# Kernel tuning notes

Hardware: AMD Instinct MI355X
Metric: run time of the kernel (lower is better)

Reference implementation:

```python
import jax, jax.numpy as jnp
import numpy as np

K_SIZE, STRIDE, PAD = 3, 2, 1

def _conv1x1(x, w, b):
    return jnp.einsum('bchw,oc->bohw', x, w) + b[None, :, None, None]

def _unfold(x, k, s, p):
    # Matches torch F.unfold ordering: channel-major, then (kh, kw). -> [B, C, k*k, L]
    B, C, H, W = x.shape
    xp = jnp.pad(x, ((0, 0), (0, 0), (p, p), (p, p)))
    ho = (H + 2 * p - k) // s + 1
    wo = (W + 2 * p - k) // s + 1
    cols = []
    for i in range(k):
        for j in range(k):
            cols.append(xp[:, :, i:i + s * (ho - 1) + 1:s, j:j + s * (wo - 1) + 1:s])
    patches = jnp.stack(cols, axis=2)            # [B, C, k*k, ho, wo]
    return patches.reshape(B, C, k * k, ho * wo)

def _forward(shallow, deep, K_w, K_b, KSA_w, KSA_b):
    B, C, H, W = shallow.shape
    d = (2 * C) // 16
    h, w = H // STRIDE, W // STRIDE
    hw = h * w
    max_out = _conv1x1(deep, KSA_w, KSA_b)            # [B, d, h, w]
    # global re-score branch
    max_out1 = jnp.max(max_out, axis=1)               # [B, h, w]
    q = max_out1.reshape(B, hw)                       # [B, hw]
    kt = max_out.reshape(B, hw, d)                    # faithful to torch .view(B,-1,d) (channel-scrambled flat view)
    lit = jnp.einsum('bp,bpd->bd', q, kt) / hw        # mean over hw of outer products -> [B, d]
    V = max_out.reshape(B, d, hw)
    re_score = jnp.einsum('bd,bdp->bp', lit, V).reshape(B, 1, h, w)
    sig = jax.nn.sigmoid(re_score)
    # local windowed attention branch
    Kx = _conv1x1(shallow, K_w, K_b)                  # [B, out, H, W]
    Kunf = _unfold(Kx, K_SIZE, STRIDE, PAD)           # [B, out, kk, hw]
    # torch does matmul([d,1],[1,kk]) then mean over d == mean_d(q_d) * K patch element
    qmean = jnp.mean(max_out, axis=1).reshape(B, 1, 1, hw)
    logits = qmean * Kunf                             # [B, out, kk, hw]
    new_kernel = jax.nn.softmax(logits, axis=2)       # softmax over window dim kk
    att = jnp.sum(new_kernel * Kunf, axis=2)          # [B, out, hw]
    att = att.reshape(B, -1, h, w)
    return sig * att + att, re_score

def setup_inputs():
    key = jax.random.key(0)
    ks = jax.random.split(key, 6)
    B, C, H, W = 4, 256, 128, 128
    out_c, d = 256, (2 * C) // 16
    return {
        'shallow': jax.random.normal(ks[0], (B, C, H, W), jnp.float32),
        'deep': jax.random.normal(ks[1], (B, 2 * C, H // 2, W // 2), jnp.float32),
        'K_w': jax.random.normal(ks[2], (out_c, C), jnp.float32) * 0.02,
        'K_b': jax.random.normal(ks[3], (out_c,), jnp.float32) * 0.02,
        'KSA_w': jax.random.normal(ks[4], (d, 2 * C), jnp.float32) * 0.02,
        'KSA_b': jax.random.normal(ks[5], (d,), jnp.float32) * 0.02,
    }

def reference(shallow, deep, K_w, K_b, KSA_w, KSA_b):
    return _forward(shallow, deep, K_w, K_b, KSA_w, KSA_b)
```

## Files before the change

kernel.cpp:

```cpp
#include <hip/hip_runtime.h>

typedef unsigned short u16;
typedef __attribute__((ext_vector_type(8))) short short8;
typedef __attribute__((ext_vector_type(4))) float float4v;
typedef __attribute__((ext_vector_type(4))) unsigned short ushort4v;

__device__ __forceinline__ u16 f2bf(float f) {
    unsigned u = __float_as_uint(f);
    u += 0x7FFFu + ((u >> 16) & 1u);
    return (u16)(u >> 16);
}
__device__ __forceinline__ float bf2f(u16 u) {
    return __uint_as_float(((unsigned)u) << 16);
}

__device__ __forceinline__ void lds_barrier() {
    asm volatile("s_waitcnt lgkmcnt(0)\n\ts_barrier" ::: "memory");
}

__device__ float g_maxout[4 * 32 * 4096];
__device__ float g_maxoutT[4 * 4096 * 32];
__device__ float g_q[16384];
__device__ float g_qmean[16384];
__device__ float g_lit[128];
__device__ float g_sigfac[16384];
__device__ u16   g_KwP[65536];
__device__ u16   g_KSAwP[16384];
__device__ u16   g_Kx[4 * 256 * 16384];

__global__ __launch_bounds__(256) void prep_kernel(
    const float* __restrict__ Kw, const float* __restrict__ KSAw)
{
    const int idx = blockIdx.x * 256 + threadIdx.x;
    if (idx < 128) g_lit[idx] = 0.f;
    if (idx < 65536) {
        const int o = idx >> 8, c = idx & 255;
        const int fi = ((o >> 4) << 3) + (c >> 5);
        const int ln = (((c >> 3) & 3) << 4) + (o & 15);
        g_KwP[fi * 512 + ln * 8 + (c & 7)] = f2bf(Kw[idx]);
    }
    if (idx < 16384) {
        const int o = idx >> 9, c = idx & 511;
        const int fi = ((c >> 5) << 1) + (o >> 4);
        const int ln = (((c >> 3) & 3) << 4) + (o & 15);
        g_KSAwP[fi * 512 + ln * 8 + (c & 7)] = f2bf(KSAw[idx]);
    }
}

__global__ __launch_bounds__(256) void gemm_deep(
    const float* __restrict__ Bias, const float* __restrict__ X)
{
    __shared__ u16 As[16384];
    const int t = threadIdx.x;
    const int wave = t >> 6, lane = t & 63;
    const int quad = lane >> 4, n16 = lane & 15;
    const int b = blockIdx.y;
    const int p = blockIdx.x * 64 + wave * 16 + n16;
    const float* Xb = X + ((long long)b << 21) + p;

#pragma unroll
    for (int i = 0; i < 8; i++)
        *(short8*)(As + ((i << 8) + t) * 8) = *(const short8*)(g_KSAwP + ((i << 8) + t) * 8);

    float xr[3][8];
#define DXLOAD(dst, kb_) { \
    const float* xp_ = Xb + ((((kb_) << 5) + (quad << 3)) << 12); \
    _Pragma("unroll") for (int j = 0; j < 8; j++) dst[j] = xp_[j << 12]; }

    DXLOAD(xr[0], 0)
    DXLOAD(xr[1], 1)
    DXLOAD(xr[2], 2)

    __syncthreads();

    float4v acc[2];
#pragma unroll
    for (int i = 0; i < 2; i++) acc[i] = (float4v){0.f, 0.f, 0.f, 0.f};

#pragma unroll
    for (int kb = 0; kb < 16; kb++) {
        short8 bfrag;
#pragma unroll
        for (int j = 0; j < 8; j++) bfrag[j] = (short)f2bf(xr[kb % 3][j]);
        if (kb < 13) DXLOAD(xr[(kb + 3) % 3], kb + 3)
#pragma unroll
        for (int ot = 0; ot < 2; ot++) {
            const short8 afrag = *(const short8*)(As + (((kb << 1) + ot) << 9) + lane * 8);
            acc[ot] = __builtin_amdgcn_mfma_f32_16x16x32_bf16(afrag, bfrag, acc[ot], 0, 0, 0);
        }
    }
#undef DXLOAD

    float mx = -3.4e38f, sm = 0.f;
#pragma unroll
    for (int ot = 0; ot < 2; ot++) {
        float4v vv;
#pragma unroll
        for (int r = 0; r < 4; r++) {
            const int o = ot * 16 + quad * 4 + r;
            vv[r] = acc[ot][r] + Bias[o];
            g_maxout[((b * 32 + o) << 12) + p] = vv[r];
            mx = fmaxf(mx, vv[r]);
            sm += vv[r];
        }
        *(float4v*)(g_maxoutT + (((b << 12) + p) << 5) + ot * 16 + quad * 4) = vv;
    }
    mx = fmaxf(mx, __shfl_xor(mx, 16, 64));
    sm += __shfl_xor(sm, 16, 64);
    mx = fmaxf(mx, __shfl_xor(mx, 32, 64));
    sm += __shfl_xor(sm, 32, 64);
    if (quad == 0) {
        g_q[(b << 12) + p] = mx;
        g_qmean[(b << 12) + p] = sm * (1.f / 32.f);
    }
}

__global__ __launch_bounds__(256) void lit_kernel()
{
    const int b = blockIdx.y;
    const int f0 = blockIdx.x * 1024;
    const int t = threadIdx.x;
    const float* mo = g_maxout + (b << 17);
    const float* qb = g_q + (b << 12);
    float acc = 0.f;
#pragma unroll
    for (int it = 0; it < 4; it++) {
        const int f = f0 + it * 256 + t;
        acc += qb[f >> 5] * mo[f];
    }
    __shared__ float red[256];
    red[t] = acc;
    __syncthreads();
    if (t < 32) {
        float s = 0.f;
#pragma unroll
        for (int k = 0; k < 8; k++) s += red[t + k * 32];
        atomicAdd(&g_lit[b * 32 + t], s * (1.f / 4096.f));
    }
}

__global__ __launch_bounds__(128) void rescore_kernel(float* __restrict__ out_re)
{
    const int idx = blockIdx.x * 128 + threadIdx.x;
    const int b = idx >> 12;
    const float4v* mt = (const float4v*)(g_maxoutT + (idx << 5));
    const float4v* lb = (const float4v*)(g_lit + b * 32);
    float r = 0.f;
#pragma unroll
    for (int j = 0; j < 8; j++) {
        const float4v m4 = mt[j];
        const float4v l4 = lb[j];
        r += m4[0] * l4[0] + m4[1] * l4[1] + m4[2] * l4[2] + m4[3] * l4[3];
    }
    out_re[idx] = r;
    g_sigfac[idx] = 1.f + 1.f / (1.f + __expf(-r));
}

__global__ __launch_bounds__(256) void gemm_kx(
    const float* __restrict__ Bias, const float* __restrict__ X)
{
    __shared__ u16 As[2][8192];
    const int t = threadIdx.x;
    const int wave = t >> 6, lane = t & 63;
    const int quad = lane >> 4, n16 = lane & 15;
    const int b = blockIdx.y;
    const int p0 = blockIdx.x * 64;
    const float* Xb = X + ((long long)b << 22) + p0 + wave * 16 + n16;

    const u16* agbase = g_KwP + wave * 16384 + lane * 8;
    const int alds = wave * 2048 + lane * 8;

    float xr[3][8];
#define XLOAD(dst, kb_) { \
    const float* xp_ = Xb + ((((kb_) << 5) + (quad << 3)) << 14); \
    _Pragma("unroll") for (int j = 0; j < 8; j++) dst[j] = xp_[j << 14]; }

    float4v acc[16];
#pragma unroll
    for (int i = 0; i < 16; i++) acc[i] = (float4v){0.f, 0.f, 0.f, 0.f};

    {
        short8 areg[4];
#pragma unroll
        for (int i = 0; i < 4; i++) areg[i] = *(const short8*)(agbase + i * 4096);
        XLOAD(xr[0], 0)
        XLOAD(xr[1], 1)
        XLOAD(xr[2], 2)
#pragma unroll
        for (int i = 0; i < 4; i++) *(short8*)(&As[0][alds + i * 512]) = areg[i];
    }
    lds_barrier();

#pragma unroll
    for (int kb = 0; kb < 8; kb++) {
        short8 areg[4];
        if (kb < 7) {
#pragma unroll
            for (int i = 0; i < 4; i++)
                areg[i] = *(const short8*)(agbase + i * 4096 + (kb + 1) * 512);
        }
        short8 bfrag;
#pragma unroll
        for (int j = 0; j < 8; j++) bfrag[j] = (short)f2bf(xr[kb % 3][j]);
        if (kb < 5) XLOAD(xr[(kb + 3) % 3], kb + 3)

        const u16* ap = &As[kb & 1][lane * 8];
#pragma unroll
        for (int ot = 0; ot < 16; ot++) {
            const short8 afrag = *(const short8*)(ap + ot * 512);
            acc[ot] = __builtin_amdgcn_mfma_f32_16x16x32_bf16(
                bfrag, afrag, acc[ot], 0, 0, 0);
        }

        if (kb < 7) {
#pragma unroll
            for (int i = 0; i < 4; i++)
                *(short8*)(&As[(kb + 1) & 1][alds + i * 512]) = areg[i];
            lds_barrier();
        }
    }
#undef XLOAD

    u16* kxb = g_Kx + (((long long)b << 8) << 14);
#pragma unroll
    for (int ot = 0; ot < 16; ot++) {
        const int o = ot * 16 + n16;
        const float bo = Bias[o];
        ushort4v w;
#pragma unroll
        for (int r = 0; r < 4; r++) w[r] = f2bf(acc[ot][r] + bo);
        *(ushort4v*)(kxb + ((long long)o << 14) + p0 + wave * 16 + (quad << 2)) = w;
    }
}

__global__ __launch_bounds__(256) void att_window(float* __restrict__ out)
{
    __shared__ u16 tile[8][9][132];
    const int t = threadIdx.x;
    const int o0 = blockIdx.y << 3, b = blockIdx.z;
    const int y0 = (blockIdx.x << 3) - 1;
    const u16* kxb = g_Kx + (((long long)b << 8) << 14);

    if (t < 72) tile[t / 9][t % 9][64] = 0;
#pragma unroll
    for (int k = 0; k < 18; k++) {
        const int e = (k << 8) + t;
        const int row = e >> 6, pr = e & 63;
        const int oi = row / 9, r = row - oi * 9;
        const int y = y0 + r;
        unsigned v = 0;
        if (y >= 0 && y < 128)
            v = *(const unsigned*)(kxb + (((long long)(o0 + oi)) << 14) + (y << 7) + (pr << 1));
        tile[oi][r][pr] = (u16)(v & 0xffffu);
        tile[oi][r][65 + pr] = (u16)(v >> 16);
    }
    __syncthreads();

    const int p = (blockIdx.x << 8) + t;
    const int pw = t & 63;
    const int rl = (t >> 6) << 1;
    const float m = g_qmean[(b << 12) + p];
    const float sf = g_sigfac[(b << 12) + p];

#pragma unroll
    for (int oi = 0; oi < 8; oi++) {
        float v[9];
#pragma unroll
        for (int ki = 0; ki < 3; ++ki) {
            v[ki * 3 + 0] = bf2f(tile[oi][rl + ki][64 + pw]);
            v[ki * 3 + 1] = bf2f(tile[oi][rl + ki][pw]);
            v[ki * 3 + 2] = bf2f(tile[oi][rl + ki][65 + pw]);
        }
        float mx = -3.4e38f;
#pragma unroll
        for (int k = 0; k < 9; ++k) mx = fmaxf(mx, m * v[k]);
        float s = 0.f, a = 0.f;
#pragma unroll
        for (int k = 0; k < 9; ++k) {
            const float e = __expf(m * v[k] - mx);
            s += e;
            a += e * v[k];
        }
        out[((((long long)b << 8) + o0 + oi) << 12) + p] = (a / s) * sf;
    }
}

extern "C" void kernel_launch(void* const* d_in, const int* in_sizes, int n_in,
                              void* d_out, int out_size, void* d_ws, size_t ws_size,
                              hipStream_t stream) {
    const float *shallow = 0, *deep = 0, *K_w = 0, *K_b = 0, *KSA_w = 0, *KSA_b = 0;
    for (int i = 0; i < n_in; ++i) {
        switch (in_sizes[i]) {
            case 16777216: shallow = (const float*)d_in[i]; break;
            case 8388608:  deep    = (const float*)d_in[i]; break;
            case 65536:    K_w     = (const float*)d_in[i]; break;
            case 256:      K_b     = (const float*)d_in[i]; break;
            case 16384:    KSA_w   = (const float*)d_in[i]; break;
            case 32:       KSA_b   = (const float*)d_in[i]; break;
        }
    }
    float* out = (float*)d_out;

    prep_kernel<<<320, 256, 0, stream>>>(K_w, KSA_w);
    gemm_deep<<<dim3(64, 4), 256, 0, stream>>>(KSA_b, deep);
    lit_kernel<<<dim3(128, 4), 256, 0, stream>>>();
    rescore_kernel<<<128, 128, 0, stream>>>(out + 4194304);
    gemm_kx<<<dim3(256, 4), 256, 0, stream>>>(K_b, shallow);
    att_window<<<dim3(16, 32, 4), 256, 0, stream>>>(out);
}
```

Measured before the change: 181.6 us.

## Stage activation tile in LDS and keep weight fragments in registers for Kx GEMM

The Kx 1x1-conv GEMM now loads the block's 64-pixel by 256-channel activation tile with float4 reads, converts it to bf16 once, and stores it in a swizzled LDS buffer. Each wave then owns 64 output channels and keeps its weight fragments in double-buffered registers loaded straight from global memory. This removes the per-k-step LDS barriers and the strided scalar global activation loads of the previous design. In exchange it needs more LDS and accumulator registers, and every wave reads weight fragments from global/L2 instead of sharing them through LDS.

Result: no change. 183.0 us (+0.8%).

```diff
diff --git a/kernel.cpp b/kernel.cpp
--- a/kernel.cpp
+++ b/kernel.cpp
@@ -12,10 +12,6 @@
 }
 __device__ __forceinline__ float bf2f(u16 u) {
     return __uint_as_float(((unsigned)u) << 16);
-}
-
-__device__ __forceinline__ void lds_barrier() {
-    asm volatile("s_waitcnt lgkmcnt(0)\n\ts_barrier" ::: "memory");
 }
 
 __device__ float g_maxout[4 * 32 * 4096];
@@ -159,77 +155,85 @@
 __global__ __launch_bounds__(256) void gemm_kx(
     const float* __restrict__ Bias, const float* __restrict__ X)
 {
-    __shared__ u16 As[2][8192];
+    __shared__ u16 Bs[16384];
     const int t = threadIdx.x;
     const int wave = t >> 6, lane = t & 63;
     const int quad = lane >> 4, n16 = lane & 15;
     const int b = blockIdx.y;
     const int p0 = blockIdx.x * 64;
-    const float* Xb = X + ((long long)b << 22) + p0 + wave * 16 + n16;
-
-    const u16* agbase = g_KwP + wave * 16384 + lane * 8;
-    const int alds = wave * 2048 + lane * 8;
-
-    float xr[3][8];
-#define XLOAD(dst, kb_) { \
-    const float* xp_ = Xb + ((((kb_) << 5) + (quad << 3)) << 14); \
-    _Pragma("unroll") for (int j = 0; j < 8; j++) dst[j] = xp_[j << 14]; }
-
-    float4v acc[16];
-#pragma unroll
-    for (int i = 0; i < 16; i++) acc[i] = (float4v){0.f, 0.f, 0.f, 0.f};
+    const float* Xb = X + ((long long)b << 22);
+
+    const u16* Ap = g_KwP + wave * 16384 + lane * 8;
+
+    short8 areg[2][4];
+#pragma unroll
+    for (int i = 0; i < 4; i++) areg[0][i] = *(const short8*)(Ap + i * 4096);
 
     {
-        short8 areg[4];
-#pragma unroll
-        for (int i = 0; i < 4; i++) areg[i] = *(const short8*)(agbase + i * 4096);
-        XLOAD(xr[0], 0)
-        XLOAD(xr[1], 1)
-        XLOAD(xr[2], 2)
-#pragma unroll
-        for (int i = 0; i < 4; i++) *(short8*)(&As[0][alds + i * 512]) = areg[i];
-    }
-    lds_barrier();
+        const int c0b = (t >> 4) << 2;
+        const int pl0 = (t & 15) << 2;
+#pragma unroll
+        for (int g = 0; g < 4; g++) {
+            const int c0 = (g << 6) + c0b;
+            float4v v[4];
+#pragma unroll
+            for (int cr = 0; cr < 4; cr++)
+                v[cr] = *(const float4v*)(Xb + ((long long)(c0 + cr) << 14) + p0 + pl0);
+#pragma unroll
+            for (int pj = 0; pj < 4; pj++) {
+                const int pl = pl0 + pj;
+                ushort4v w;
+#pragma unroll
+                for (int cr = 0; cr < 4; cr++) w[cr] = f2bf(v[cr][pj]);
+                *(ushort4v*)(Bs + (pl << 8) + (c0 ^ ((pl & 7) << 3))) = w;
+            }
+        }
+    }
+
+    float4v acc[4][4];
+#pragma unroll
+    for (int i = 0; i < 4; i++)
+#pragma unroll
+        for (int j = 0; j < 4; j++) acc[i][j] = (float4v){0.f, 0.f, 0.f, 0.f};
+
+    __syncthreads();
 
 #pragma unroll
     for (int kb = 0; kb < 8; kb++) {
-        short8 areg[4];
+        const int cr = kb & 1;
         if (kb < 7) {
 #pragma unroll
             for (int i = 0; i < 4; i++)
-                areg[i] = *(const short8*)(agbase + i * 4096 + (kb + 1) * 512);
-        }
-        short8 bfrag;
-#pragma unroll
-        for (int j = 0; j < 8; j++) bfrag[j] = (short)f2bf(xr[kb % 3][j]);
-        if (kb < 5) XLOAD(xr[(kb + 3) % 3], kb + 3)
-
-        const u16* ap = &As[kb & 1][lane * 8];
-#pragma unroll
-        for (int ot = 0; ot < 16; ot++) {
-            const short8 afrag = *(const short8*)(ap + ot * 512);
-            acc[ot] = __builtin_amdgcn_mfma_f32_16x16x32_bf16(
-                bfrag, afrag, acc[ot], 0, 0, 0);
-        }
-
-        if (kb < 7) {
+                areg[cr ^ 1][i] = *(const short8*)(Ap + i * 4096 + (kb + 1) * 512);
+        }
+        short8 bf[4];
+#pragma unroll
+        for (int pg = 0; pg < 4; pg++) {
+            const int pl = (pg << 4) + n16;
+            const int c0 = (kb << 5) + (quad << 3);
+            bf[pg] = *(const short8*)(Bs + (pl << 8) + (c0 ^ ((pl & 7) << 3)));
+        }
+#pragma unroll
+        for (int pg = 0; pg < 4; pg++)
 #pragma unroll
             for (int i = 0; i < 4; i++)
-                *(short8*)(&As[(kb + 1) & 1][alds + i * 512]) = areg[i];
-            lds_barrier();
-        }
-    }
-#undef XLOAD
+                acc[pg][i] = __builtin_amdgcn_mfma_f32_16x16x32_bf16(
+                    bf[pg], areg[cr][i], acc[pg][i], 0, 0, 0);
+    }
 
     u16* kxb = g_Kx + (((long long)b << 8) << 14);
 #pragma unroll
-    for (int ot = 0; ot < 16; ot++) {
-        const int o = ot * 16 + n16;
+    for (int i = 0; i < 4; i++) {
+        const int o = wave * 64 + i * 16 + n16;
         const float bo = Bias[o];
-        ushort4v w;
-#pragma unroll
-        for (int r = 0; r < 4; r++) w[r] = f2bf(acc[ot][r] + bo);
-        *(ushort4v*)(kxb + ((long long)o << 14) + p0 + wave * 16 + (quad << 2)) = w;
+        u16* orow = kxb + ((long long)o << 14) + p0 + (quad << 2);
+#pragma unroll
+        for (int pg = 0; pg < 4; pg++) {
+            ushort4v w;
+#pragma unroll
+            for (int r = 0; r < 4; r++) w[r] = f2bf(acc[pg][i][r] + bo);
+            *(ushort4v*)(orow + (pg << 4)) = w;
+        }
     }
 }
 
```
